# Performance work log

Measured on AMD Instinct MI355X. Metric: run time of the kernel, lower is better.

The kernel has to match this reference:

```python
import jax, jax.numpy as jnp
import numpy as np

N, E, D, H, C, L = 50000, 600000, 128, 128, 64, 3
LN_EPS = 1e-5


def setup_inputs() -> dict:
    key = jax.random.key(0)
    ks = jax.random.split(key, 6)
    x = jax.random.normal(ks[0], (N, D), jnp.float32)
    edge_index = jax.random.randint(ks[1], (2, E), 0, N, jnp.int32)
    Wg = jax.random.normal(ks[2], (L, D, H), jnp.float32) * (1.0 / np.sqrt(D))
    bg = jnp.zeros((L, H), jnp.float32)
    ln_g = jnp.ones((L, H), jnp.float32)
    ln_b = jnp.zeros((L, H), jnp.float32)
    mlp_W1 = jax.random.normal(ks[3], (D + L * H, H), jnp.float32) * (1.0 / np.sqrt(D + L * H))
    mlp_b1 = jnp.zeros((H,), jnp.float32)
    mlp_W2 = jax.random.normal(ks[4], (H, C), jnp.float32) * (1.0 / np.sqrt(H))
    mlp_b2 = jnp.zeros((C,), jnp.float32)
    return {"x": x, "edge_index": edge_index, "Wg": Wg, "bg": bg,
            "ln_g": ln_g, "ln_b": ln_b, "mlp_W1": mlp_W1, "mlp_b1": mlp_b1,
            "mlp_W2": mlp_W2, "mlp_b2": mlp_b2}


def _layer_norm(h, g, b):
    mu = jnp.mean(h, axis=-1, keepdims=True)
    var = jnp.mean((h - mu) ** 2, axis=-1, keepdims=True)
    return g * (h - mu) * jax.lax.rsqrt(var + LN_EPS) + b


def _gcn(h, W, b, src, dst, dinv):
    # GCNConv with added self-loops and symmetric normalization:
    # out = D^{-1/2} (A + I) D^{-1/2} (h W) + b
    hW = h @ W                                   # [N, H]
    coef = (dinv[src] * dinv[dst])[:, None]      # [E, 1]
    agg = jax.ops.segment_sum(hW[src] * coef, dst, num_segments=N)
    agg = agg + hW * (dinv * dinv)[:, None]      # self-loop term
    return agg + b


def reference(x, edge_index, Wg, bg, ln_g, ln_b, mlp_W1, mlp_b1, mlp_W2, mlp_b2):
    src, dst = edge_index[0], edge_index[1]
    # degree including self-loop
    deg = jnp.ones((N,), x.dtype).at[dst].add(1.0)
    dinv = jax.lax.rsqrt(deg)
    feats = [x]
    h = x
    for i in range(L):  # small fixed layer count
        h = _gcn(h, Wg[i], bg[i], src, dst, dinv)
        h = _layer_norm(h, ln_g[i], ln_b[i])
        h = jax.nn.relu(h)
        feats.append(h)
    xc = jnp.concatenate(feats, axis=1)          # [N, D + L*H]
    z = jax.nn.relu(xc @ mlp_W1 + mlp_b1)
    z = z @ mlp_W2 + mlp_b2
    return jax.nn.softmax(z, axis=1)
```

## Files before the change

### kernel.cpp

```cpp
#include <hip/hip_runtime.h>
#include <math.h>

#define D 128
#define HH 128
#define CC 64
#define NLAYERS 3
#define LN_EPS 1e-5f

typedef __attribute__((ext_vector_type(8))) short bf16x8;
typedef __attribute__((ext_vector_type(4))) float f32x4;
typedef unsigned short u16;
typedef unsigned int u32;

__device__ __forceinline__ u16 f2bf(float f) {
    u32 u = __float_as_uint(f);
    u32 r = u + 0x7FFFu + ((u >> 16) & 1u);
    return (u16)(r >> 16);
}
__device__ __forceinline__ float bf2f(u16 h) {
    return __uint_as_float(((u32)h) << 16);
}


__global__ void k_zero_cnt(int* __restrict__ cnt, int n) {
    int i = blockIdx.x * blockDim.x + threadIdx.x;
    if (i < n) cnt[i] = 0;
}

__global__ void k_count(const int* __restrict__ dst, int* __restrict__ cnt, int E) {
    int i = blockIdx.x * blockDim.x + threadIdx.x;
    if (i < E) atomicAdd(&cnt[dst[i]], 1);
}

__global__ void k_dinv(const int* __restrict__ cnt, float* __restrict__ dinv, int N) {
    int i = blockIdx.x * blockDim.x + threadIdx.x;
    if (i < N) dinv[i] = rsqrtf(1.0f + (float)cnt[i]);
}

__global__ void k_scan_a(const int* __restrict__ cnt, int* __restrict__ rowptr,
                         int* __restrict__ bsum, int N) {
    __shared__ int s[1024];
    int tid = threadIdx.x;
    int i = blockIdx.x * 1024 + tid;
    int v = (i < N) ? cnt[i] : 0;
    s[tid] = v;
    __syncthreads();
    for (int off = 1; off < 1024; off <<= 1) {
        int t = (tid >= off) ? s[tid - off] : 0;
        __syncthreads();
        s[tid] += t;
        __syncthreads();
    }
    if (i < N) rowptr[i] = s[tid] - v;
    if (tid == 1023) bsum[blockIdx.x] = s[tid];
}

__global__ void k_scan_b(int* __restrict__ bsum, int nb) {
    int t = threadIdx.x;
    int v = (t < nb) ? bsum[t] : 0;
    int incl = v;
    for (int off = 1; off < 64; off <<= 1) {
        int u = __shfl_up(incl, off, 64);
        if (t >= off) incl += u;
    }
    if (t < nb) bsum[t] = incl - v;
}

__global__ void k_scan_c(int* __restrict__ rowptr, const int* __restrict__ bsum,
                         int* __restrict__ cursor, int N, int E) {
    int i = blockIdx.x * blockDim.x + threadIdx.x;
    if (i < N) {
        int v = rowptr[i] + bsum[i >> 10];
        rowptr[i] = v;
        cursor[i] = v;
    }
    if (i == 0) rowptr[N] = E;
}

__global__ void k_scatter(const int* __restrict__ src, const int* __restrict__ dst,
                          const float* __restrict__ dinv,
                          int* __restrict__ cursor, int2* __restrict__ ecol, int E) {
    int i = blockIdx.x * blockDim.x + threadIdx.x;
    if (i < E) {
        int s = src[i], d = dst[i];
        int p = atomicAdd(&cursor[d], 1);
        float c = dinv[s] * dinv[d];
        ecol[p] = make_int2(s, __float_as_int(c));
    }
}


__global__ void k_split_x(const float* __restrict__ x, u16* __restrict__ xh,
                          u16* __restrict__ xl, int total) {
    int i = blockIdx.x * blockDim.x + threadIdx.x;
    if (i >= total) return;
    int row = i >> 7, c = i & 127;
    float v = x[i];
    u16 h = f2bf(v);
    u16 l = f2bf(v - bf2f(h));
    xh[(size_t)row * 512 + c] = h;
    xl[(size_t)row * 128 + c] = l;
}

__global__ void k_tile_w(const float* __restrict__ W, u16* __restrict__ th,
                         u16* __restrict__ tl, int KN, int nshift) {
    int idx = blockIdx.x * blockDim.x + threadIdx.x;
    if (idx >= KN) return;
    int k = idx >> nshift, n = idx & ((1 << nshift) - 1);
    int kc = k >> 5, q = (k >> 3) & 3, j = k & 7;
    float v = W[idx];
    u16 h = f2bf(v);
    int o = (((kc * 4 + q) << nshift) + n) * 8 + j;
    th[o] = h;
    if (tl) tl[o] = f2bf(v - bf2f(h));
}

template <bool SPLIT2>
__global__ __launch_bounds__(256) void k_gemm_lf(
    const u16* __restrict__ Ahi, int strideA, int colOff,
    const u16* __restrict__ Alo, int strideAlo,
    const u16* __restrict__ Bt, u16* __restrict__ OUTb, int N)
{
    const int tid  = threadIdx.x;
    const int lane = tid & 63;
    const int wave = tid >> 6;
    const int wr   = wave & 1;
    const int wc   = wave >> 1;
    const int quad = lane >> 4;
    const int l15  = lane & 15;
    const int row0 = blockIdx.x * 64;

    const u16* pAh[2];
    const u16* pAl[2];
    #pragma unroll
    for (int i = 0; i < 2; ++i) {
        int r = row0 + wr * 32 + i * 16 + l15;
        if (r >= N) r = N - 1;
        pAh[i] = Ahi + (size_t)r * strideA + colOff + quad * 8;
        if (SPLIT2) pAl[i] = Alo + (size_t)r * strideAlo + quad * 8;
    }
    const u16* pB = Bt + ((size_t)quad * 128 + wc * 64 + l15) * 8;

    bf16x8 ah[4][2], al[4][2], bh[4][4];
    #pragma unroll
    for (int kc = 0; kc < 4; ++kc) {
        #pragma unroll
        for (int i = 0; i < 2; ++i) {
            ah[kc][i] = *(const bf16x8*)(pAh[i] + kc * 32);
            if (SPLIT2) al[kc][i] = *(const bf16x8*)(pAl[i] + kc * 32);
        }
        #pragma unroll
        for (int j = 0; j < 4; ++j)
            bh[kc][j] = *(const bf16x8*)(pB + (size_t)kc * 4096 + j * 128);
    }

    f32x4 acc[2][4];
    #pragma unroll
    for (int i = 0; i < 2; ++i)
        #pragma unroll
        for (int j = 0; j < 4; ++j)
            #pragma unroll
            for (int r = 0; r < 4; ++r) acc[i][j][r] = 0.f;

    #pragma unroll
    for (int kc = 0; kc < 4; ++kc)
        #pragma unroll
        for (int i = 0; i < 2; ++i)
            #pragma unroll
            for (int j = 0; j < 4; ++j) {
                acc[i][j] = __builtin_amdgcn_mfma_f32_16x16x32_bf16(ah[kc][i], bh[kc][j], acc[i][j], 0, 0, 0);
                if (SPLIT2)
                    acc[i][j] = __builtin_amdgcn_mfma_f32_16x16x32_bf16(al[kc][i], bh[kc][j], acc[i][j], 0, 0, 0);
            }

    #pragma unroll
    for (int i = 0; i < 2; ++i)
        #pragma unroll
        for (int j = 0; j < 4; ++j) {
            int col = wc * 64 + j * 16 + l15;
            #pragma unroll
            for (int r = 0; r < 4; ++r) {
                int grow = row0 + wr * 32 + i * 16 + quad * 4 + r;
                if (grow < N)
                    OUTb[(size_t)grow * 128 + col] = f2bf(acc[i][j][r]);
            }
        }
}

__global__ __launch_bounds__(256) void k_mlp_fused(
    const u16* __restrict__ xcH, const u16* __restrict__ xl,
    const u16* __restrict__ B1t, const float* __restrict__ b1,
    const u16* __restrict__ W2h, const u16* __restrict__ W2l,
    const float* __restrict__ b2, float* __restrict__ out, int N)
{
    __shared__ u16 sZh[32 * 128];
    __shared__ u16 sZl[32 * 128];

    const int tid  = threadIdx.x;
    const int lane = tid & 63;
    const int wave = tid >> 6;
    const int wr   = wave & 1;
    const int wc   = wave >> 1;
    const int quad = lane >> 4;
    const int l15  = lane & 15;
    const int row0 = blockIdx.x * 32;

    int arow = row0 + wr * 16 + l15;
    if (arow >= N) arow = N - 1;
    const u16* pAx = xcH + (size_t)arow * 512 + quad * 8;
    const u16* pAl = xl  + (size_t)arow * 128 + quad * 8;
    const u16* pB  = B1t + ((size_t)quad * 128 + wc * 64 + l15) * 8;

    f32x4 acc[4];
    #pragma unroll
    for (int j = 0; j < 4; ++j)
        #pragma unroll
        for (int r = 0; r < 4; ++r) acc[j][r] = 0.f;

    bf16x8 abuf[3], bbuf[3][4];
    #define LOADI(i, s)                                                          \
        {                                                                        \
            const int bk = ((i) < 16) ? (i) : ((i) - 16);                        \
            abuf[s] = ((i) < 16) ? *(const bf16x8*)(pAx + (i) * 32)              \
                                 : *(const bf16x8*)(pAl + ((i) - 16) * 32);      \
            _Pragma("unroll")                                                    \
            for (int j = 0; j < 4; ++j)                                          \
                bbuf[s][j] = *(const bf16x8*)(pB + (size_t)bk * 4096 + j * 128); \
        }
    LOADI(0, 0)
    LOADI(1, 1)
    #pragma unroll
    for (int i = 0; i < 20; ++i) {
        if (i + 2 < 20) {
            const int s = (i + 2) % 3;
            LOADI(i + 2, s)
        }
        const int u = i % 3;
        #pragma unroll
        for (int j = 0; j < 4; ++j)
            acc[j] = __builtin_amdgcn_mfma_f32_16x16x32_bf16(abuf[u], bbuf[u][j], acc[j], 0, 0, 0);
    }
    #undef LOADI

    #pragma unroll
    for (int jt = 0; jt < 4; ++jt) {
        int col = wc * 64 + jt * 16 + l15;
        float bv = b1[col];
        int qq = col >> 3, jj = col & 7;
        #pragma unroll
        for (int rr = 0; rr < 4; ++rr) {
            int r = wr * 16 + quad * 4 + rr;
            float v = fmaxf(acc[jt][rr] + bv, 0.f);
            u16 h = f2bf(v);
            sZh[(qq * 32 + r) * 8 + jj] = h;
            sZl[(qq * 32 + r) * 8 + jj] = f2bf(v - bf2f(h));
        }
    }
    __syncthreads();

    if (wave < 2) {
        f32x4 oacc[4];
        #pragma unroll
        for (int j = 0; j < 4; ++j)
            #pragma unroll
            for (int r = 0; r < 4; ++r) oacc[j][r] = 0.f;

        #pragma unroll
        for (int kc = 0; kc < 4; ++kc) {
            int qq = kc * 4 + quad;
            bf16x8 zh = *(const bf16x8*)&sZh[(qq * 32 + wave * 16 + l15) * 8];
            bf16x8 zl = *(const bf16x8*)&sZl[(qq * 32 + wave * 16 + l15) * 8];
            #pragma unroll
            for (int jt = 0; jt < 4; ++jt) {
                int n = jt * 16 + l15;
                bf16x8 wh = *(const bf16x8*)&W2h[(qq * 64 + n) * 8];
                bf16x8 wl = *(const bf16x8*)&W2l[(qq * 64 + n) * 8];
                oacc[jt] = __builtin_amdgcn_mfma_f32_16x16x32_bf16(zh, wh, oacc[jt], 0, 0, 0);
                oacc[jt] = __builtin_amdgcn_mfma_f32_16x16x32_bf16(zh, wl, oacc[jt], 0, 0, 0);
                oacc[jt] = __builtin_amdgcn_mfma_f32_16x16x32_bf16(zl, wh, oacc[jt], 0, 0, 0);
            }
        }

        #pragma unroll
        for (int jt = 0; jt < 4; ++jt) {
            float bv = b2[jt * 16 + l15];
            #pragma unroll
            for (int r = 0; r < 4; ++r) oacc[jt][r] += bv;
        }
        #pragma unroll
        for (int r = 0; r < 4; ++r) {
            float m = fmaxf(fmaxf(oacc[0][r], oacc[1][r]), fmaxf(oacc[2][r], oacc[3][r]));
            #pragma unroll
            for (int mask = 8; mask; mask >>= 1) m = fmaxf(m, __shfl_xor(m, mask, 64));
            float p0 = __expf(oacc[0][r] - m);
            float p1 = __expf(oacc[1][r] - m);
            float p2 = __expf(oacc[2][r] - m);
            float p3 = __expf(oacc[3][r] - m);
            float s = p0 + p1 + p2 + p3;
            #pragma unroll
            for (int mask = 8; mask; mask >>= 1) s += __shfl_xor(s, mask, 64);
            float inv = 1.0f / s;
            int grow = row0 + wave * 16 + quad * 4 + r;
            if (grow < N) {
                float* o = out + (size_t)grow * CC + l15;
                o[0]  = p0 * inv;
                o[16] = p1 * inv;
                o[32] = p2 * inv;
                o[48] = p3 * inv;
            }
        }
    }
}

__global__ __launch_bounds__(256, 8) void k_agg_ln(
    const u16* __restrict__ hWb,
    const int* __restrict__ rowptr, const int2* __restrict__ ecol,
    const float* __restrict__ dinv,
    const float* __restrict__ bg, const float* __restrict__ g,
    const float* __restrict__ b,
    u16* __restrict__ outHi, int N)
{
    const int lane = threadIdx.x & 63;
    const int f0 = lane * 2;

    const float bgx = bg[f0], bgy = bg[f0 + 1];
    const float gx  = g[f0],  gy  = g[f0 + 1];
    const float bx  = b[f0],  by  = b[f0 + 1];

    const int nwaves = gridDim.x * 4;
    for (int wid = blockIdx.x * 4 + (threadIdx.x >> 6); wid < N; wid += nwaves) {
        float di = dinv[wid];
        float sc = di * di;

        u32 hv = *(const u32*)(hWb + (size_t)wid * HH + f0);
        float ax  = bf2f((u16)hv) * sc;
        float ay  = bf2f((u16)(hv >> 16)) * sc;
        float ax1 = 0.f, ay1 = 0.f, ax2 = 0.f, ay2 = 0.f, ax3 = 0.f, ay3 = 0.f;

        int e0 = rowptr[wid];
        int e1 = rowptr[wid + 1];
        int e = e0;
        for (; e + 4 <= e1; e += 4) {
            int2 p0 = ecol[e];
            int2 p1 = ecol[e + 1];
            int2 p2 = ecol[e + 2];
            int2 p3 = ecol[e + 3];
            u32 v0 = *(const u32*)(hWb + (size_t)p0.x * HH + f0);
            u32 v1 = *(const u32*)(hWb + (size_t)p1.x * HH + f0);
            u32 v2 = *(const u32*)(hWb + (size_t)p2.x * HH + f0);
            u32 v3 = *(const u32*)(hWb + (size_t)p3.x * HH + f0);
            float c0 = __int_as_float(p0.y);
            float c1 = __int_as_float(p1.y);
            float c2 = __int_as_float(p2.y);
            float c3 = __int_as_float(p3.y);
            ax  += bf2f((u16)v0) * c0;  ay  += bf2f((u16)(v0 >> 16)) * c0;
            ax1 += bf2f((u16)v1) * c1;  ay1 += bf2f((u16)(v1 >> 16)) * c1;
            ax2 += bf2f((u16)v2) * c2;  ay2 += bf2f((u16)(v2 >> 16)) * c2;
            ax3 += bf2f((u16)v3) * c3;  ay3 += bf2f((u16)(v3 >> 16)) * c3;
        }
        for (; e < e1; ++e) {
            int2 p = ecol[e];
            u32 v = *(const u32*)(hWb + (size_t)p.x * HH + f0);
            float c = __int_as_float(p.y);
            ax += bf2f((u16)v) * c;
            ay += bf2f((u16)(v >> 16)) * c;
        }
        ax += ax1 + ax2 + ax3;
        ay += ay1 + ay2 + ay3;
        ax += bgx;
        ay += bgy;

        float ssum = ax + ay;
        #pragma unroll
        for (int off = 32; off; off >>= 1) ssum += __shfl_xor(ssum, off, 64);
        float mu = ssum * (1.0f / 128.0f);
        float dx = ax - mu, dy = ay - mu;
        float vsum = dx * dx + dy * dy;
        #pragma unroll
        for (int off = 32; off; off >>= 1) vsum += __shfl_xor(vsum, off, 64);
        float rstd = rsqrtf(vsum * (1.0f / 128.0f) + LN_EPS);

        float ox = fmaxf(gx * dx * rstd + bx, 0.f);
        float oy = fmaxf(gy * dy * rstd + by, 0.f);

        *(u32*)&outHi[(size_t)wid * 512 + f0] = (u32)f2bf(ox) | ((u32)f2bf(oy) << 16);
    }
}

extern "C" void kernel_launch(void* const* d_in, const int* in_sizes, int n_in,
                              void* d_out, int out_size, void* d_ws, size_t ws_size,
                              hipStream_t stream) {
    const float* x   = (const float*)d_in[0];
    const int*   ei  = (const int*)  d_in[1];
    const float* Wg  = (const float*)d_in[2];
    const float* bg  = (const float*)d_in[3];
    const float* lng = (const float*)d_in[4];
    const float* lnb = (const float*)d_in[5];
    const float* W1  = (const float*)d_in[6];
    const float* b1  = (const float*)d_in[7];
    const float* W2  = (const float*)d_in[8];
    const float* b2  = (const float*)d_in[9];
    float* out = (float*)d_out;

    const int N = in_sizes[0] / D;
    const int E = in_sizes[1] / 2;
    const int* srcp = ei;
    const int* dstp = ei + E;

    char* ws = (char*)d_ws;
    size_t off = 0;
    auto alloc = [&](size_t bytes) -> void* {
        void* p = ws + off;
        off += (bytes + 511) & ~(size_t)511;
        return p;
    };
    int*   cnt    = (int*)  alloc((size_t)N * 4);
    int*   rowptr = (int*)  alloc((size_t)(N + 1) * 4);
    int*   cursor = (int*)  alloc((size_t)N * 4);
    int*   bsum   = (int*)  alloc(64 * 4);
    int2*  ecol   = (int2*) alloc((size_t)E * 8);
    float* dinv   = (float*)alloc((size_t)N * 4);
    u16*   hWb    = (u16*)  alloc((size_t)N * HH * 2);
    u16*   xcH    = (u16*)  alloc((size_t)N * 512 * 2);
    u16*   xl     = (u16*)  alloc((size_t)N * 128 * 2);
    u16*   WgtH   = (u16*)  alloc((size_t)NLAYERS * D * HH * 2);
    u16*   W1tH   = (u16*)  alloc((size_t)(D + NLAYERS * HH) * HH * 2);
    u16*   W2tH   = (u16*)  alloc((size_t)HH * CC * 2);
    u16*   W2tL   = (u16*)  alloc((size_t)HH * CC * 2);

    const int B = 256;
    const int gN = (N + B - 1) / B;
    const int gE = (E + B - 1) / B;
    const int nsb = (N + 1023) / 1024;

    k_zero_cnt<<<gN, B, 0, stream>>>(cnt, N);
    k_count<<<gE, B, 0, stream>>>(dstp, cnt, E);
    k_dinv<<<gN, B, 0, stream>>>(cnt, dinv, N);
    k_scan_a<<<nsb, 1024, 0, stream>>>(cnt, rowptr, bsum, N);
    k_scan_b<<<1, 64, 0, stream>>>(bsum, nsb);
    k_scan_c<<<gN, B, 0, stream>>>(rowptr, bsum, cursor, N, E);
    k_scatter<<<gE, B, 0, stream>>>(srcp, dstp, dinv, cursor, ecol, E);

    k_split_x<<<(N * D + B - 1) / B, B, 0, stream>>>(x, xcH, xl, N * D);
    for (int l = 0; l < NLAYERS; ++l)
        k_tile_w<<<(D * HH + B - 1) / B, B, 0, stream>>>(Wg + (size_t)l * D * HH,
                                                         WgtH + (size_t)l * D * HH,
                                                         nullptr, D * HH, 7);
    k_tile_w<<<((D + NLAYERS * HH) * HH + B - 1) / B, B, 0, stream>>>(W1, W1tH, nullptr,
                                                                      (D + NLAYERS * HH) * HH, 7);
    k_tile_w<<<(HH * CC + B - 1) / B, B, 0, stream>>>(W2, W2tH, W2tL, HH * CC, 6);

    const int gemmBlocks = (N + 63) / 64;
    const int mlpBlocks  = (N + 31) / 32;
    const int aggBlocks  = 2048;

    for (int l = 0; l < NLAYERS; ++l) {
        if (l == 0)
            k_gemm_lf<true><<<gemmBlocks, B, 0, stream>>>(xcH, 512, 0, xl, 128,
                                                          WgtH, hWb, N);
        else
            k_gemm_lf<false><<<gemmBlocks, B, 0, stream>>>(xcH, 512, l * HH, nullptr, 0,
                                                           WgtH + (size_t)l * D * HH, hWb, N);
        k_agg_ln<<<aggBlocks, B, 0, stream>>>(hWb, rowptr, ecol, dinv,
                                              bg + (size_t)l * HH,
                                              lng + (size_t)l * HH,
                                              lnb + (size_t)l * HH,
                                              xcH + (size_t)(l + 1) * HH, N);
    }

    k_mlp_fused<<<mlpBlocks, B, 0, stream>>>(xcH, xl, W1tH, b1,
                                             W2tH, W2tL, b2, out, N);
}
```

Before: 356.3 us.

## Widen MLP tile to 64 rows, unroll edge gather by 8, fold dinv into scan

```diff
diff --git a/kernel.cpp b/kernel.cpp
--- a/kernel.cpp
+++ b/kernel.cpp
@@ -30,11 +30,6 @@
 __global__ void k_count(const int* __restrict__ dst, int* __restrict__ cnt, int E) {
     int i = blockIdx.x * blockDim.x + threadIdx.x;
     if (i < E) atomicAdd(&cnt[dst[i]], 1);
-}
-
-__global__ void k_dinv(const int* __restrict__ cnt, float* __restrict__ dinv, int N) {
-    int i = blockIdx.x * blockDim.x + threadIdx.x;
-    if (i < N) dinv[i] = rsqrtf(1.0f + (float)cnt[i]);
 }
 
 __global__ void k_scan_a(const int* __restrict__ cnt, int* __restrict__ rowptr,
@@ -67,12 +62,14 @@
 }
 
 __global__ void k_scan_c(int* __restrict__ rowptr, const int* __restrict__ bsum,
+                         const int* __restrict__ cnt, float* __restrict__ dinv,
                          int* __restrict__ cursor, int N, int E) {
     int i = blockIdx.x * blockDim.x + threadIdx.x;
     if (i < N) {
         int v = rowptr[i] + bsum[i >> 10];
         rowptr[i] = v;
         cursor[i] = v;
+        dinv[i] = rsqrtf(1.0f + (float)cnt[i]);
     }
     if (i == 0) rowptr[N] = E;
 }
@@ -193,8 +190,8 @@
     const u16* __restrict__ W2h, const u16* __restrict__ W2l,
     const float* __restrict__ b2, float* __restrict__ out, int N)
 {
-    __shared__ u16 sZh[32 * 128];
-    __shared__ u16 sZl[32 * 128];
+    __shared__ u16 sZh[64 * 128];
+    __shared__ u16 sZl[64 * 128];
 
     const int tid  = threadIdx.x;
     const int lane = tid & 63;
@@ -203,42 +200,55 @@
     const int wc   = wave >> 1;
     const int quad = lane >> 4;
     const int l15  = lane & 15;
-    const int row0 = blockIdx.x * 32;
-
-    int arow = row0 + wr * 16 + l15;
-    if (arow >= N) arow = N - 1;
-    const u16* pAx = xcH + (size_t)arow * 512 + quad * 8;
-    const u16* pAl = xl  + (size_t)arow * 128 + quad * 8;
-    const u16* pB  = B1t + ((size_t)quad * 128 + wc * 64 + l15) * 8;
-
-    f32x4 acc[4];
-    #pragma unroll
-    for (int j = 0; j < 4; ++j)
-        #pragma unroll
-        for (int r = 0; r < 4; ++r) acc[j][r] = 0.f;
-
-    bf16x8 abuf[3], bbuf[3][4];
+    const int row0 = blockIdx.x * 64;
+
+    const u16* pAh[2];
+    const u16* pAl[2];
+    #pragma unroll
+    for (int f = 0; f < 2; ++f) {
+        int r = row0 + wr * 32 + f * 16 + l15;
+        if (r >= N) r = N - 1;
+        pAh[f] = xcH + (size_t)r * 512 + quad * 8;
+        pAl[f] = xl  + (size_t)r * 128 + quad * 8;
+    }
+    const u16* pB = B1t + ((size_t)quad * 128 + wc * 64 + l15) * 8;
+
+    f32x4 acc[2][4];
+    #pragma unroll
+    for (int f = 0; f < 2; ++f)
+        #pragma unroll
+        for (int j = 0; j < 4; ++j)
+            #pragma unroll
+            for (int r = 0; r < 4; ++r) acc[f][j][r] = 0.f;
+
+    bf16x8 abuf[4][2], bbuf[4][4];
     #define LOADI(i, s)                                                          \
         {                                                                        \
             const int bk = ((i) < 16) ? (i) : ((i) - 16);                        \
-            abuf[s] = ((i) < 16) ? *(const bf16x8*)(pAx + (i) * 32)              \
-                                 : *(const bf16x8*)(pAl + ((i) - 16) * 32);      \
+            _Pragma("unroll")                                                    \
+            for (int f = 0; f < 2; ++f)                                          \
+                abuf[s][f] = ((i) < 16)                                          \
+                    ? *(const bf16x8*)(pAh[f] + (i) * 32)                        \
+                    : *(const bf16x8*)(pAl[f] + ((i) - 16) * 32);                \
             _Pragma("unroll")                                                    \
             for (int j = 0; j < 4; ++j)                                          \
                 bbuf[s][j] = *(const bf16x8*)(pB + (size_t)bk * 4096 + j * 128); \
         }
     LOADI(0, 0)
     LOADI(1, 1)
+    LOADI(2, 2)
     #pragma unroll
     for (int i = 0; i < 20; ++i) {
-        if (i + 2 < 20) {
-            const int s = (i + 2) % 3;
-            LOADI(i + 2, s)
-        }
-        const int u = i % 3;
-        #pragma unroll
-        for (int j = 0; j < 4; ++j)
-            acc[j] = __builtin_amdgcn_mfma_f32_16x16x32_bf16(abuf[u], bbuf[u][j], acc[j], 0, 0, 0);
+        if (i + 3 < 20) {
+            const int s = (i + 3) & 3;
+            LOADI(i + 3, s)
+        }
+        const int u = i & 3;
+        #pragma unroll
+        for (int f = 0; f < 2; ++f)
+            #pragma unroll
+            for (int j = 0; j < 4; ++j)
+                acc[f][j] = __builtin_amdgcn_mfma_f32_16x16x32_bf16(abuf[u][f], bbuf[u][j], acc[f][j], 0, 0, 0);
     }
     #undef LOADI
 
@@ -248,66 +258,67 @@
         float bv = b1[col];
         int qq = col >> 3, jj = col & 7;
         #pragma unroll
-        for (int rr = 0; rr < 4; ++rr) {
-            int r = wr * 16 + quad * 4 + rr;
-            float v = fmaxf(acc[jt][rr] + bv, 0.f);
-            u16 h = f2bf(v);
-            sZh[(qq * 32 + r) * 8 + jj] = h;
-            sZl[(qq * 32 + r) * 8 + jj] = f2bf(v - bf2f(h));
+        for (int f = 0; f < 2; ++f) {
+            #pragma unroll
+            for (int rr = 0; rr < 4; ++rr) {
+                int r = wr * 32 + f * 16 + quad * 4 + rr;
+                float v = fmaxf(acc[f][jt][rr] + bv, 0.f);
+                u16 h = f2bf(v);
+                sZh[(qq * 64 + r) * 8 + jj] = h;
+                sZl[(qq * 64 + r) * 8 + jj] = f2bf(v - bf2f(h));
+            }
         }
     }
     __syncthreads();
 
-    if (wave < 2) {
-        f32x4 oacc[4];
-        #pragma unroll
-        for (int j = 0; j < 4; ++j)
-            #pragma unroll
-            for (int r = 0; r < 4; ++r) oacc[j][r] = 0.f;
-
-        #pragma unroll
-        for (int kc = 0; kc < 4; ++kc) {
-            int qq = kc * 4 + quad;
-            bf16x8 zh = *(const bf16x8*)&sZh[(qq * 32 + wave * 16 + l15) * 8];
-            bf16x8 zl = *(const bf16x8*)&sZl[(qq * 32 + wave * 16 + l15) * 8];
-            #pragma unroll
-            for (int jt = 0; jt < 4; ++jt) {
-                int n = jt * 16 + l15;
-                bf16x8 wh = *(const bf16x8*)&W2h[(qq * 64 + n) * 8];
-                bf16x8 wl = *(const bf16x8*)&W2l[(qq * 64 + n) * 8];
-                oacc[jt] = __builtin_amdgcn_mfma_f32_16x16x32_bf16(zh, wh, oacc[jt], 0, 0, 0);
-                oacc[jt] = __builtin_amdgcn_mfma_f32_16x16x32_bf16(zh, wl, oacc[jt], 0, 0, 0);
-                oacc[jt] = __builtin_amdgcn_mfma_f32_16x16x32_bf16(zl, wh, oacc[jt], 0, 0, 0);
-            }
-        }
-
+    f32x4 oacc[4];
+    #pragma unroll
+    for (int j = 0; j < 4; ++j)
+        #pragma unroll
+        for (int r = 0; r < 4; ++r) oacc[j][r] = 0.f;
+
+    #pragma unroll
+    for (int kc = 0; kc < 4; ++kc) {
+        int qq = kc * 4 + quad;
+        bf16x8 zh = *(const bf16x8*)&sZh[(qq * 64 + wave * 16 + l15) * 8];
+        bf16x8 zl = *(const bf16x8*)&sZl[(qq * 64 + wave * 16 + l15) * 8];
         #pragma unroll
         for (int jt = 0; jt < 4; ++jt) {
-            float bv = b2[jt * 16 + l15];
-            #pragma unroll
-            for (int r = 0; r < 4; ++r) oacc[jt][r] += bv;
-        }
-        #pragma unroll
-        for (int r = 0; r < 4; ++r) {
-            float m = fmaxf(fmaxf(oacc[0][r], oacc[1][r]), fmaxf(oacc[2][r], oacc[3][r]));
-            #pragma unroll
-            for (int mask = 8; mask; mask >>= 1) m = fmaxf(m, __shfl_xor(m, mask, 64));
-            float p0 = __expf(oacc[0][r] - m);
-            float p1 = __expf(oacc[1][r] - m);
-            float p2 = __expf(oacc[2][r] - m);
-            float p3 = __expf(oacc[3][r] - m);
-            float s = p0 + p1 + p2 + p3;
-            #pragma unroll
-            for (int mask = 8; mask; mask >>= 1) s += __shfl_xor(s, mask, 64);
-            float inv = 1.0f / s;
-            int grow = row0 + wave * 16 + quad * 4 + r;
-            if (grow < N) {
-                float* o = out + (size_t)grow * CC + l15;
-                o[0]  = p0 * inv;
-                o[16] = p1 * inv;
-                o[32] = p2 * inv;
-                o[48] = p3 * inv;
-            }
+            int n = jt * 16 + l15;
+            bf16x8 wh = *(const bf16x8*)&W2h[(qq * 64 + n) * 8];
+            bf16x8 wl = *(const bf16x8*)&W2l[(qq * 64 + n) * 8];
+            oacc[jt] = __builtin_amdgcn_mfma_f32_16x16x32_bf16(zh, wh, oacc[jt], 0, 0, 0);
+            oacc[jt] = __builtin_amdgcn_mfma_f32_16x16x32_bf16(zh, wl, oacc[jt], 0, 0, 0);
+            oacc[jt] = __builtin_amdgcn_mfma_f32_16x16x32_bf16(zl, wh, oacc[jt], 0, 0, 0);
+        }
+    }
+
+    #pragma unroll
+    for (int jt = 0; jt < 4; ++jt) {
+        float bv = b2[jt * 16 + l15];
+        #pragma unroll
+        for (int r = 0; r < 4; ++r) oacc[jt][r] += bv;
+    }
+    #pragma unroll
+    for (int r = 0; r < 4; ++r) {
+        float m = fmaxf(fmaxf(oacc[0][r], oacc[1][r]), fmaxf(oacc[2][r], oacc[3][r]));
+        #pragma unroll
+        for (int mask = 8; mask; mask >>= 1) m = fmaxf(m, __shfl_xor(m, mask, 64));
+        float p0 = __expf(oacc[0][r] - m);
+        float p1 = __expf(oacc[1][r] - m);
+        float p2 = __expf(oacc[2][r] - m);
+        float p3 = __expf(oacc[3][r] - m);
+        float s = p0 + p1 + p2 + p3;
+        #pragma unroll
+        for (int mask = 8; mask; mask >>= 1) s += __shfl_xor(s, mask, 64);
+        float inv = 1.0f / s;
+        int grow = row0 + wave * 16 + quad * 4 + r;
+        if (grow < N) {
+            float* o = out + (size_t)grow * CC + l15;
+            o[0]  = p0 * inv;
+            o[16] = p1 * inv;
+            o[32] = p2 * inv;
+            o[48] = p3 * inv;
         }
     }
 }
@@ -340,6 +351,27 @@
         int e0 = rowptr[wid];
         int e1 = rowptr[wid + 1];
         int e = e0;
+        for (; e + 8 <= e1; e += 8) {
+            int2 p[8];
+            u32  v[8];
+            #pragma unroll
+            for (int t = 0; t < 8; ++t) p[t] = ecol[e + t];
+            #pragma unroll
+            for (int t = 0; t < 8; ++t)
+                v[t] = *(const u32*)(hWb + (size_t)p[t].x * HH + f0);
+            #pragma unroll
+            for (int t = 0; t < 8; ++t) {
+                float c = __int_as_float(p[t].y);
+                float vx = bf2f((u16)v[t]) * c;
+                float vy = bf2f((u16)(v[t] >> 16)) * c;
+                switch (t & 3) {
+                    case 0: ax  += vx; ay  += vy; break;
+                    case 1: ax1 += vx; ay1 += vy; break;
+                    case 2: ax2 += vx; ay2 += vy; break;
+                    default: ax3 += vx; ay3 += vy; break;
+                }
+            }
+        }
         for (; e + 4 <= e1; e += 4) {
             int2 p0 = ecol[e];
             int2 p1 = ecol[e + 1];
@@ -349,14 +381,10 @@
             u32 v1 = *(const u32*)(hWb + (size_t)p1.x * HH + f0);
             u32 v2 = *(const u32*)(hWb + (size_t)p2.x * HH + f0);
             u32 v3 = *(const u32*)(hWb + (size_t)p3.x * HH + f0);
-            float c0 = __int_as_float(p0.y);
-            float c1 = __int_as_float(p1.y);
-            float c2 = __int_as_float(p2.y);
-            float c3 = __int_as_float(p3.y);
-            ax  += bf2f((u16)v0) * c0;  ay  += bf2f((u16)(v0 >> 16)) * c0;
-            ax1 += bf2f((u16)v1) * c1;  ay1 += bf2f((u16)(v1 >> 16)) * c1;
-            ax2 += bf2f((u16)v2) * c2;  ay2 += bf2f((u16)(v2 >> 16)) * c2;
-            ax3 += bf2f((u16)v3) * c3;  ay3 += bf2f((u16)(v3 >> 16)) * c3;
+            ax  += bf2f((u16)v0) * __int_as_float(p0.y);  ay  += bf2f((u16)(v0 >> 16)) * __int_as_float(p0.y);
+            ax1 += bf2f((u16)v1) * __int_as_float(p1.y);  ay1 += bf2f((u16)(v1 >> 16)) * __int_as_float(p1.y);
+            ax2 += bf2f((u16)v2) * __int_as_float(p2.y);  ay2 += bf2f((u16)(v2 >> 16)) * __int_as_float(p2.y);
+            ax3 += bf2f((u16)v3) * __int_as_float(p3.y);  ay3 += bf2f((u16)(v3 >> 16)) * __int_as_float(p3.y);
         }
         for (; e < e1; ++e) {
             int2 p = ecol[e];
@@ -435,10 +463,9 @@
 
     k_zero_cnt<<<gN, B, 0, stream>>>(cnt, N);
     k_count<<<gE, B, 0, stream>>>(dstp, cnt, E);
-    k_dinv<<<gN, B, 0, stream>>>(cnt, dinv, N);
     k_scan_a<<<nsb, 1024, 0, stream>>>(cnt, rowptr, bsum, N);
     k_scan_b<<<1, 64, 0, stream>>>(bsum, nsb);
-    k_scan_c<<<gN, B, 0, stream>>>(rowptr, bsum, cursor, N, E);
+    k_scan_c<<<gN, B, 0, stream>>>(rowptr, bsum, cnt, dinv, cursor, N, E);
     k_scatter<<<gE, B, 0, stream>>>(srcp, dstp, dinv, cursor, ecol, E);
 
     k_split_x<<<(N * D + B - 1) / B, B, 0, stream>>>(x, xcH, xl, N * D);
@@ -451,7 +478,6 @@
     k_tile_w<<<(HH * CC + B - 1) / B, B, 0, stream>>>(W2, W2tH, W2tL, HH * CC, 6);
 
     const int gemmBlocks = (N + 63) / 64;
-    const int mlpBlocks  = (N + 31) / 32;
     const int aggBlocks  = 2048;
 
     for (int l = 0; l < NLAYERS; ++l) {
@@ -468,6 +494,6 @@
                                               xcH + (size_t)(l + 1) * HH, N);
     }
 
-    k_mlp_fused<<<mlpBlocks, B, 0, stream>>>(xcH, xl, W1tH, b1,
-                                             W2tH, W2tL, b2, out, N);
-}
+    k_mlp_fused<<<gemmBlocks, B, 0, stream>>>(xcH, xl, W1tH, b1,
+                                              W2tH, W2tL, b2, out, N);
+}
```

After: 346.8 us. 2.7% less time.
